# Performance work log

Hardware: AMD Instinct MI355X
Metric: run time of the kernel (lower is better)

Reference implementation:

```python
import jax, jax.numpy as jnp
import numpy as np

B, S, H, NH, HD = 2, 2048, 2048, 16, 128
E, TOPK, I = 8, 2, 2048
EPS = 1e-5
ROPE_THETA = 10000.0


def setup_inputs() -> dict:
    key = jax.random.key(0)
    ks = jax.random.split(key, 11)
    s = 0.02
    return {
        "hidden_states": jax.random.normal(ks[0], (B, S, H), jnp.float32),
        "position_ids": jnp.broadcast_to(jnp.arange(S, dtype=jnp.int32), (B, S)),
        "rms1_w": jnp.ones((H,), jnp.float32),
        "rms2_w": jnp.ones((H,), jnp.float32),
        "q_w": jax.random.normal(ks[1], (H, H), jnp.float32) * s,
        "k_w": jax.random.normal(ks[2], (H, H), jnp.float32) * s,
        "v_w": jax.random.normal(ks[3], (H, H), jnp.float32) * s,
        "o_w": jax.random.normal(ks[4], (H, H), jnp.float32) * s,
        "router_w": jax.random.normal(ks[5], (H, E), jnp.float32) * s,
        "w1": jax.random.normal(ks[6], (E, H, I), jnp.float32) * s,
        "w2": jax.random.normal(ks[7], (E, I, H), jnp.float32) * s,
        "w3": jax.random.normal(ks[8], (E, H, I), jnp.float32) * s,
    }


def rmsnorm(x, w):
    var = jnp.mean(x * x, axis=-1, keepdims=True)
    return (x * jax.lax.rsqrt(var + EPS)) * w


def rope(x, pos):
    # x: [B,S,NH,HD], pos: [B,S]
    half = HD // 2
    inv_freq = 1.0 / (ROPE_THETA ** (jnp.arange(0, half, dtype=jnp.float32) / half))
    ang = pos.astype(jnp.float32)[..., None] * inv_freq  # [B,S,half]
    cos = jnp.cos(ang)[:, :, None, :]
    sin = jnp.sin(ang)[:, :, None, :]
    x1, x2 = x[..., :half], x[..., half:]
    return jnp.concatenate([x1 * cos - x2 * sin, x2 * cos + x1 * sin], axis=-1)


def attention(x, pos, q_w, k_w, v_w, o_w):
    q = (x @ q_w).reshape(B, S, NH, HD)
    k = (x @ k_w).reshape(B, S, NH, HD)
    v = (x @ v_w).reshape(B, S, NH, HD)
    q = rope(q, pos)
    k = rope(k, pos)
    scores = jnp.einsum("bqhd,bkhd->bhqk", q, k) / np.sqrt(HD).astype(np.float32)
    causal = jnp.tril(jnp.ones((S, S), bool))
    scores = jnp.where(causal, scores, jnp.finfo(scores.dtype).min)
    probs = jax.nn.softmax(scores, axis=-1)
    ctx = jnp.einsum("bhqk,bkhd->bqhd", probs, v).reshape(B, S, H)
    return ctx @ o_w


def moe(x, router_w, w1, w2, w3):
    t = x.reshape(B * S, H)
    probs = jax.nn.softmax(t @ router_w, axis=-1)  # [T,E]
    top_v, top_i = jax.lax.top_k(probs, TOPK)
    top_v = top_v / jnp.sum(top_v, axis=-1, keepdims=True)
    T = B * S
    coeff = jnp.zeros((T, E), x.dtype).at[jnp.arange(T)[:, None], top_i].set(top_v)
    y = jnp.zeros((T, H), x.dtype)
    for e in range(E):  # fixed small expert loop
        h = jax.nn.silu(t @ w1[e]) * (t @ w3[e])
        y = y + coeff[:, e:e + 1] * (h @ w2[e])
    return y.reshape(B, S, H)


def reference(hidden_states, position_ids, rms1_w, rms2_w, q_w, k_w, v_w, o_w,
              router_w, w1, w2, w3):
    residual = hidden_states
    h = rmsnorm(hidden_states, rms1_w).astype(hidden_states.dtype)
    h = attention(h, position_ids, q_w, k_w, v_w, o_w)
    h = residual + h
    residual = h
    h = rmsnorm(h, rms2_w).astype(h.dtype)
    h = moe(h, router_w, w1, w2, w3)
    return residual + h
```

## Files before the change

### kernel.cpp

```cpp
#include <hip/hip_runtime.h>
#include <hip/hip_bf16.h>

constexpr int CB   = 2;
constexpr int CS   = 2048;
constexpr int CH   = 2048;
constexpr int CNH  = 16;
constexpr int CHD  = 128;
constexpr int CE   = 8;
constexpr int CI   = 2048;
constexpr int CT   = CB * CS;
constexpr int CQKV = 3 * CH;

typedef __attribute__((ext_vector_type(8))) short short8;
typedef __attribute__((ext_vector_type(4))) float float4v;
typedef __attribute__((ext_vector_type(4))) unsigned short ushort4v;
typedef unsigned int uint32;

__device__ __forceinline__ float bf2f(unsigned short u) {
    union { unsigned int i; float f; } x; x.i = ((unsigned int)u) << 16; return x.f;
}
__device__ __forceinline__ unsigned short f2bf(float f) {
    union { float f; unsigned int i; } x; x.f = f;
    unsigned int r = x.i + 0x7fffu + ((x.i >> 16) & 1u);
    return (unsigned short)(r >> 16);
}
__device__ __forceinline__ uint32 packpair(uint32 r0, uint32 r1) {
    return __builtin_amdgcn_perm(r1, r0, 0x07060302u);
}
__device__ __forceinline__ uint32 rnebits(float f) {
    uint32 u = __float_as_uint(f);
    return u + 0x7fffu + ((u >> 16) & 1u);
}
__device__ __forceinline__ void split2(float f0, float f1, uint32& h, uint32& l) {
    uint32 r0 = rnebits(f0), r1 = rnebits(f1);
    h = packpair(r0, r1);
    float d0 = f0 - __uint_as_float(r0 & 0xffff0000u);
    float d1 = f1 - __uint_as_float(r1 & 0xffff0000u);
    l = packpair(rnebits(d0), rnebits(d1));
}
__device__ __forceinline__ void rne16_store(const float* fv, unsigned short* dst) {
    uint32 h[8];
    #pragma unroll
    for (int p = 0; p < 8; p++) h[p] = packpair(rnebits(fv[2 * p]), rnebits(fv[2 * p + 1]));
    ((uint4*)dst)[0] = make_uint4(h[0], h[1], h[2], h[3]);
    ((uint4*)dst)[1] = make_uint4(h[4], h[5], h[6], h[7]);
}
__device__ __forceinline__ void gl16(const void* g, void* l) {
    __builtin_amdgcn_global_load_lds(
        (const __attribute__((address_space(1))) void*)g,
        (__attribute__((address_space(3))) void*)l, 16, 0, 0);
}

__global__ __launch_bounds__(256) void rmsnorm_k(const float* __restrict__ x,
                                                 const float* __restrict__ w,
                                                 unsigned short* __restrict__ o1,
                                                 unsigned short* __restrict__ o2) {
    const int row = blockIdx.x;
    const float* xr = x + (size_t)row * CH;
    const int base = threadIdx.x * 8;
    float4 v0 = *(const float4*)(xr + base);
    float4 v1 = *(const float4*)(xr + base + 4);
    float ss = v0.x*v0.x + v0.y*v0.y + v0.z*v0.z + v0.w*v0.w
             + v1.x*v1.x + v1.y*v1.y + v1.z*v1.z + v1.w*v1.w;
    #pragma unroll
    for (int o = 1; o < 64; o <<= 1) ss += __shfl_xor(ss, o);
    __shared__ float ps[4];
    if ((threadIdx.x & 63) == 0) ps[threadIdx.x >> 6] = ss;
    __syncthreads();
    const float scale = rsqrtf((ps[0] + ps[1] + ps[2] + ps[3]) / (float)CH + 1e-5f);
    float4 w0 = *(const float4*)(w + base);
    float4 w1 = *(const float4*)(w + base + 4);
    float r[8] = {v0.x * scale * w0.x, v0.y * scale * w0.y, v0.z * scale * w0.z, v0.w * scale * w0.w,
                  v1.x * scale * w1.x, v1.y * scale * w1.y, v1.z * scale * w1.z, v1.w * scale * w1.w};
    uint32 h[4], l[4];
    #pragma unroll
    for (int p = 0; p < 4; p++) split2(r[2 * p], r[2 * p + 1], h[p], l[p]);
    *(uint4*)(o1 + (size_t)row * CH + base) = make_uint4(h[0], h[1], h[2], h[3]);
    *(uint4*)(o2 + (size_t)row * CH + base) = make_uint4(l[0], l[1], l[2], l[3]);
}

__global__ __launch_bounds__(256) void rmsrouter_k(const float* __restrict__ x,
                                                   const float* __restrict__ w,
                                                   const float* __restrict__ rw,
                                                   unsigned short* __restrict__ h2,
                                                   int* __restrict__ cnt,
                                                   int* __restrict__ tok,
                                                   float* __restrict__ gate) {
    const int row = blockIdx.x;
    const float* xr = x + (size_t)row * CH;
    const int base = threadIdx.x * 8;
    float4 v0 = *(const float4*)(xr + base);
    float4 v1 = *(const float4*)(xr + base + 4);
    float ss = v0.x*v0.x + v0.y*v0.y + v0.z*v0.z + v0.w*v0.w
             + v1.x*v1.x + v1.y*v1.y + v1.z*v1.z + v1.w*v1.w;
    #pragma unroll
    for (int o = 1; o < 64; o <<= 1) ss += __shfl_xor(ss, o);
    __shared__ float ps[4];
    __shared__ double dacc[4][8];
    const int wave = threadIdx.x >> 6, lane = threadIdx.x & 63;
    if (lane == 0) ps[wave] = ss;
    __syncthreads();
    const float scale = rsqrtf((ps[0] + ps[1] + ps[2] + ps[3]) / (float)CH + 1e-5f);
    float4 w0 = *(const float4*)(w + base);
    float4 w1 = *(const float4*)(w + base + 4);
    float r[8] = {v0.x * scale * w0.x, v0.y * scale * w0.y, v0.z * scale * w0.z, v0.w * scale * w0.w,
                  v1.x * scale * w1.x, v1.y * scale * w1.y, v1.z * scale * w1.z, v1.w * scale * w1.w};
    rne16_store(r, h2 + (size_t)row * CH + base);
    const float vv[8] = {v0.x, v0.y, v0.z, v0.w, v1.x, v1.y, v1.z, v1.w};
    const float ww[8] = {w0.x, w0.y, w0.z, w0.w, w1.x, w1.y, w1.z, w1.w};
    double acc[8] = {0, 0, 0, 0, 0, 0, 0, 0};
    #pragma unroll
    for (int jj = 0; jj < 8; jj++) {
        const double xn = (double)vv[jj] * (double)ww[jj];
        const float* rr = rw + (size_t)(base + jj) * CE;
        #pragma unroll
        for (int e = 0; e < 8; e++) acc[e] += xn * (double)rr[e];
    }
    #pragma unroll
    for (int e = 0; e < 8; e++) {
        #pragma unroll
        for (int o = 1; o < 64; o <<= 1) acc[e] += __shfl_xor(acc[e], o);
    }
    if (lane == 0) {
        #pragma unroll
        for (int e = 0; e < 8; e++) dacc[wave][e] = acc[e];
    }
    __syncthreads();
    if (threadIdx.x == 0) {
        double a[8];
        #pragma unroll
        for (int e = 0; e < 8; e++) a[e] = dacc[0][e] + dacc[1][e] + dacc[2][e] + dacc[3][e];
        int e0 = 0;
        #pragma unroll
        for (int e = 1; e < 8; e++) if (a[e] > a[e0]) e0 = e;
        int e1 = (e0 == 0) ? 1 : 0;
        #pragma unroll
        for (int e = 0; e < 8; e++) if (e != e0 && a[e] > a[e1]) e1 = e;
        const double dl = (double)scale * (a[e1] - a[e0]);
        const double p1r = exp(dl);
        const float g0 = (float)(1.0 / (1.0 + p1r));
        const float g1 = (float)(p1r / (1.0 + p1r));
        int pos0 = atomicAdd(&cnt[e0], 1);
        tok[e0 * 4096 + pos0] = row; gate[e0 * 4096 + pos0] = g0;
        int pos1 = atomicAdd(&cnt[e1], 1);
        tok[e1 * 4096 + pos1] = row; gate[e1 * 4096 + pos1] = g1;
    }
}

__global__ void rope_tab_k(float2* __restrict__ tab) {
    int i = blockIdx.x * 256 + threadIdx.x;
    int p = i >> 6, j = i & 63;
    double inv = pow(10000.0, -(double)j / 64.0);
    float invf = (float)inv;
    float angf = (float)p * invf;
    double da = (double)angf;
    tab[i] = make_float2((float)cos(da), (float)sin(da));
}

__global__ __launch_bounds__(256) void rope_k(unsigned short* __restrict__ qh,
                                              unsigned short* __restrict__ ql,
                                              const int* __restrict__ pos,
                                              const float2* __restrict__ tab) {
    int i = blockIdx.x * 256 + threadIdx.x;
    if (i >= CT * CNH * 8) return;
    int t = i >> 7, r = i & 127, hh = r >> 3, jo = (r & 7) << 3;
    const float2* tp = tab + (size_t)pos[t] * 64 + jo;
    float4 tc0 = ((const float4*)tp)[0];
    float4 tc1 = ((const float4*)tp)[1];
    float4 tc2 = ((const float4*)tp)[2];
    float4 tc3 = ((const float4*)tp)[3];
    float cx[8] = {tc0.x, tc0.z, tc1.x, tc1.z, tc2.x, tc2.z, tc3.x, tc3.z};
    float cy[8] = {tc0.y, tc0.w, tc1.y, tc1.w, tc2.y, tc2.w, tc3.y, tc3.w};
    const size_t off = (size_t)t * CQKV + hh * CHD + jo;
    #pragma unroll
    for (int s = 0; s < 2; s++) {
        unsigned short* hp = qh + off + s * CH;
        unsigned short* lp = ql + off + s * CH;
        short8 x1h = *(short8*)hp,        x1l = *(short8*)lp;
        short8 x2h = *(short8*)(hp + 64), x2l = *(short8*)(lp + 64);
        const unsigned short* p1h = (const unsigned short*)&x1h;
        const unsigned short* p1l = (const unsigned short*)&x1l;
        const unsigned short* p2h = (const unsigned short*)&x2h;
        const unsigned short* p2l = (const unsigned short*)&x2l;
        short8 y1h, y1l, y2h, y2l;
        unsigned short* q1h = (unsigned short*)&y1h;
        unsigned short* q1l = (unsigned short*)&y1l;
        unsigned short* q2h = (unsigned short*)&y2h;
        unsigned short* q2l = (unsigned short*)&y2l;
        #pragma unroll
        for (int jj = 0; jj < 8; jj++) {
            const float x1 = bf2f(p1h[jj]) + bf2f(p1l[jj]);
            const float x2 = bf2f(p2h[jj]) + bf2f(p2l[jj]);
            const float yy1 = x1 * cx[jj] - x2 * cy[jj];
            const float yy2 = x2 * cx[jj] + x1 * cy[jj];
            const uint32 r1 = rnebits(yy1), r2 = rnebits(yy2);
            q1h[jj] = (unsigned short)(r1 >> 16);
            q2h[jj] = (unsigned short)(r2 >> 16);
            q1l[jj] = f2bf(yy1 - __uint_as_float(r1 & 0xffff0000u));
            q2l[jj] = f2bf(yy2 - __uint_as_float(r2 & 0xffff0000u));
        }
        *(short8*)hp        = y1h;
        *(short8*)(hp + 64) = y2h;
        *(short8*)lp        = y1l;
        *(short8*)(lp + 64) = y2l;
    }
}

template<int NMAT>
__global__ __launch_bounds__(256) void conv_k(const float* __restrict__ S0,
                                              const float* __restrict__ S1,
                                              unsigned short* __restrict__ D) {
    __shared__ float t[64][65];
    const int n0 = blockIdx.x * 64, k0 = blockIdx.y * 64, e = blockIdx.z;
    const size_t esrc = (size_t)e * 2048 * 2048;
    const int cc = threadIdx.x & 63, r4 = threadIdx.x >> 6;
    const int nl = threadIdx.x >> 2, q = threadIdx.x & 3;
    #pragma unroll
    for (int s = 0; s < NMAT; s++) {
        const float* S = s ? S1 : S0;
        __syncthreads();
        #pragma unroll
        for (int j = 0; j < 16; j++) {
            const int row = j * 4 + r4;
            t[cc][row] = S[esrc + (size_t)(k0 + row) * 2048 + n0 + cc];
        }
        __syncthreads();
        const int orow = (NMAT == 2) ? (2 * (n0 + nl) + s) : (n0 + nl);
        unsigned short* dp = D + (size_t)e * (NMAT * 2048) * 2048 + (size_t)orow * 2048 + k0 + q * 16;
        float fv[16];
        #pragma unroll
        for (int j = 0; j < 16; j++) fv[j] = t[nl][q * 16 + j];
        rne16_store(fv, dp);
    }
}

template<int NMAT>
__global__ __launch_bounds__(256) void convs_k(const float* __restrict__ S0,
                                               const float* __restrict__ S1,
                                               const float* __restrict__ S2,
                                               unsigned short* __restrict__ Dh,
                                               unsigned short* __restrict__ Dl) {
    __shared__ float t[64][65];
    const int n0 = blockIdx.x * 64, k0 = blockIdx.y * 64, z = blockIdx.z;
    const float* S = S0;
    if (NMAT == 3) S = (z == 0) ? S0 : ((z == 1) ? S1 : S2);
    const int cc = threadIdx.x & 63, r4 = threadIdx.x >> 6;
    #pragma unroll
    for (int j = 0; j < 16; j++) {
        const int row = j * 4 + r4;
        t[cc][row] = S[(size_t)(k0 + row) * 2048 + n0 + cc];
    }
    __syncthreads();
    const int nl = threadIdx.x >> 2, q = threadIdx.x & 3;
    float fv[16];
    #pragma unroll
    for (int j = 0; j < 16; j++) fv[j] = t[nl][q * 16 + j];
    uint32 h[8], l[8];
    #pragma unroll
    for (int p = 0; p < 8; p++) split2(fv[2 * p], fv[2 * p + 1], h[p], l[p]);
    const size_t off = (size_t)(z * 2048 + n0 + nl) * 2048 + k0 + q * 16;
    ((uint4*)(Dh + off))[0] = make_uint4(h[0], h[1], h[2], h[3]);
    ((uint4*)(Dh + off))[1] = make_uint4(h[4], h[5], h[6], h[7]);
    ((uint4*)(Dl + off))[0] = make_uint4(l[0], l[1], l[2], l[3]);
    ((uint4*)(Dl + off))[1] = make_uint4(l[4], l[5], l[6], l[7]);
}

template<int MODE>
__global__ __launch_bounds__(256) void sgemm_k(
    const unsigned short* __restrict__ Ahg, const unsigned short* __restrict__ Alg, int lda,
    const unsigned short* __restrict__ Bhg, const unsigned short* __restrict__ Blg, int K,
    unsigned short* __restrict__ Ch, unsigned short* __restrict__ Cl,
    float* __restrict__ Cf, int ldc,
    const float* __restrict__ resid, float* __restrict__ C2) {
    __shared__ unsigned short AhS[128 * 32], AlS[128 * 32], BhS[128 * 32], BlS[128 * 32];
    const int mt = blockIdx.x, nt = blockIdx.y, tid = threadIdx.x;
    const int m0 = mt * 128;
    const int wave = tid >> 6, lane = tid & 63;
    const int lr = lane & 15, lg = lane >> 4;
    const int wr = (tid >> 7) & 1, wc = (tid >> 6) & 1;
    const int sr = lane >> 2;
    const int sc = (lane & 3) * 8;
    const int r0 = wave * 32;
    const unsigned short* gAh = Ahg + (size_t)(m0 + r0 + sr) * lda + sc;
    const unsigned short* gAl = Alg + (size_t)(m0 + r0 + sr) * lda + sc;
    const unsigned short* gBh = Bhg + (size_t)(nt * 128 + r0 + sr) * K + sc;
    const unsigned short* gBl = Blg + (size_t)(nt * 128 + r0 + sr) * K + sc;
    const size_t rstepA = (size_t)16 * lda, rstepB = (size_t)16 * K;
    unsigned short* lAh = AhS + r0 * 32;
    unsigned short* lAl = AlS + r0 * 32;
    unsigned short* lBh = BhS + r0 * 32;
    unsigned short* lBl = BlS + r0 * 32;

    float4v acc[4][4];
    #pragma unroll
    for (int m = 0; m < 4; m++)
        #pragma unroll
        for (int n = 0; n < 4; n++) acc[m][n] = (float4v){0.f, 0.f, 0.f, 0.f};

    for (int k0 = 0; k0 < K; k0 += 32) {
        __syncthreads();
        gl16(gAh + k0, lAh);            gl16(gAh + k0 + rstepA, lAh + 512);
        gl16(gAl + k0, lAl);            gl16(gAl + k0 + rstepA, lAl + 512);
        gl16(gBh + k0, lBh);            gl16(gBh + k0 + rstepB, lBh + 512);
        gl16(gBl + k0, lBl);            gl16(gBl + k0 + rstepB, lBl + 512);
        __syncthreads();
        short8 fah[4], fal[4], fbh[4], fbl[4];
        #pragma unroll
        for (int m = 0; m < 4; m++) {
            fah[m] = *(const short8*)(AhS + (wr * 64 + m * 16 + lr) * 32 + lg * 8);
            fal[m] = *(const short8*)(AlS + (wr * 64 + m * 16 + lr) * 32 + lg * 8);
        }
        #pragma unroll
        for (int n = 0; n < 4; n++) {
            fbh[n] = *(const short8*)(BhS + (wc * 64 + n * 16 + lr) * 32 + lg * 8);
            fbl[n] = *(const short8*)(BlS + (wc * 64 + n * 16 + lr) * 32 + lg * 8);
        }
        #pragma unroll
        for (int n = 0; n < 4; n++)
            #pragma unroll
            for (int m = 0; m < 4; m++) {
                acc[m][n] = __builtin_amdgcn_mfma_f32_16x16x32_bf16(fal[m], fbh[n], acc[m][n], 0, 0, 0);
                acc[m][n] = __builtin_amdgcn_mfma_f32_16x16x32_bf16(fah[m], fbl[n], acc[m][n], 0, 0, 0);
                acc[m][n] = __builtin_amdgcn_mfma_f32_16x16x32_bf16(fah[m], fbh[n], acc[m][n], 0, 0, 0);
            }
    }
    #pragma unroll
    for (int m = 0; m < 4; m++) {
        const int rb = wr * 64 + m * 16 + (lane >> 4) * 4;
        #pragma unroll
        for (int n = 0; n < 4; n++) {
            const int ccol = nt * 128 + wc * 64 + n * 16 + lr;
            #pragma unroll
            for (int r = 0; r < 4; r++) {
                const size_t idx = (size_t)(m0 + rb + r) * ldc + ccol;
                if (MODE == 1) {
                    const float v = acc[m][n][r] + resid[idx];
                    Cf[idx] = v;
                    C2[idx] = v;
                } else {
                    const float v = acc[m][n][r];
                    uint32 rr = rnebits(v);
                    Ch[idx] = (unsigned short)(rr >> 16);
                    Cl[idx] = f2bf(v - __uint_as_float(rr & 0xffff0000u));
                }
            }
        }
    }
}

template<int MODE>
__global__ __launch_bounds__(256) void gemm_k(
    const unsigned short* __restrict__ A, int lda,
    const unsigned short* __restrict__ Bt, int K, int Ne,
    void* __restrict__ Cp, int ldc,
    const int* __restrict__ cnt, const int* __restrict__ tokl,
    const float* __restrict__ gatel, const int* __restrict__ pb) {
    __shared__ unsigned short As[128 * 32];
    __shared__ unsigned short Bs[128 * 32];
    const int nt = blockIdx.x, mt = blockIdx.y, e = blockIdx.z;
    const int m0 = mt * 128;
    const int c = cnt[e];
    if (m0 >= c) return;
    const int valid = (c - m0 < 128) ? (c - m0) : 128;
    const int tid = threadIdx.x;
    const int wave = tid >> 6, lane = tid & 63;
    const int lr = lane & 15;
    const int wr = (tid >> 7) & 1, wc = (tid >> 6) & 1;
    const int sr = lane >> 2, sc = (lane & 3) * 8;
    const int r0 = wave * 32;
    size_t gr0, gr1;
    {
        int ra = r0 + sr, rb2 = r0 + 16 + sr;
        if (MODE == 2) {
            ra = ra < valid ? ra : valid - 1;
            rb2 = rb2 < valid ? rb2 : valid - 1;
            gr0 = (size_t)tokl[e * 4096 + m0 + ra];
            gr1 = (size_t)tokl[e * 4096 + m0 + rb2];
        } else {
            int x0 = m0 + ra, x1 = m0 + rb2;
            gr0 = (size_t)(pb[e] + (x0 < c ? x0 : c - 1));
            gr1 = (size_t)(pb[e] + (x1 < c ? x1 : c - 1));
        }
    }
    const unsigned short* gA0 = A + gr0 * (size_t)lda + sc;
    const unsigned short* gA1 = A + gr1 * (size_t)lda + sc;
    const unsigned short* gB = Bt + (size_t)e * Ne * K + (size_t)(nt * 128 + r0 + sr) * K + sc;
    const size_t rstepB = (size_t)16 * K;
    unsigned short* lA = As + r0 * 32;
    unsigned short* lB = Bs + r0 * 32;

    float4v acc[4][4];
    #pragma unroll
    for (int m = 0; m < 4; m++)
        #pragma unroll
        for (int n = 0; n < 4; n++) acc[m][n] = (float4v){0.f, 0.f, 0.f, 0.f};

    for (int k0 = 0; k0 < K; k0 += 32) {
        __syncthreads();
        gl16(gA0 + k0, lA);             gl16(gA1 + k0, lA + 512);
        gl16(gB + k0, lB);              gl16(gB + k0 + rstepB, lB + 512);
        __syncthreads();
        short8 af[4], bf[4];
        const int lg = lane >> 4;
        #pragma unroll
        for (int m = 0; m < 4; m++) af[m] = *(const short8*)(As + (wr * 64 + m * 16 + lr) * 32 + lg * 8);
        #pragma unroll
        for (int n = 0; n < 4; n++) bf[n] = *(const short8*)(Bs + (wc * 64 + n * 16 + lr) * 32 + lg * 8);
        #pragma unroll
        for (int n = 0; n < 4; n++)
            #pragma unroll
            for (int m = 0; m < 4; m++)
                acc[m][n] = __builtin_amdgcn_mfma_f32_16x16x32_bf16(af[m], bf[n], acc[m][n], 0, 0, 0);
    }

    #pragma unroll
    for (int m = 0; m < 4; m++) {
        const int rb = wr * 64 + m * 16 + (lane >> 4) * 4;
        #pragma unroll
        for (int n = 0; n < 4; n++) {
            const int col = nt * 128 + wc * 64 + n * 16 + lr;
            #pragma unroll
            for (int r = 0; r < 4; r++) {
                const int row = rb + r;
                const float v = acc[m][n][r];
                if (MODE == 2) {
                    const float other = __shfl_xor(v, 1);
                    if (!(lr & 1) && row < valid) {
                        const float g1 = v, g3 = other;
                        const float hsw = (g1 / (1.f + __expf(-g1))) * g3;
                        ((unsigned short*)Cp)[(size_t)(pb[e] + m0 + row) * ldc + (col >> 1)] = f2bf(hsw);
                    }
                } else {
                    if (row < valid) {
                        const int t = tokl[e * 4096 + m0 + row];
                        const float g = gatel[e * 4096 + m0 + row];
                        atomicAdd(((float*)Cp) + (size_t)t * ldc + col, v * g);
                    }
                }
            }
        }
    }
}

__global__ __launch_bounds__(256) void attn_k(const unsigned short* __restrict__ qh,
                                              const unsigned short* __restrict__ ql,
                                              unsigned short* __restrict__ ch,
                                              unsigned short* __restrict__ cl) {
    __shared__ unsigned short Ksh[32][136], Ksl[32][136];
    __shared__ unsigned short Vth[128][40], Vtl[128][40];
    const int bid = blockIdx.x;
    const int xcd = bid & 7, jj = bid >> 3;
    const int bh  = xcd * 4 + (jj >> 5);
    const int qb  = 31 - (jj & 31);
    const int h   = bh & 15, b = bh >> 4;
    const int tid = threadIdx.x;
    const int wave = tid >> 6, lane = tid & 63, lr = lane & 15, lg = lane >> 4;
    const size_t tb = (size_t)b * CS;
    const int q0 = qb * 64 + wave * 16;

    short8 qfh[4], qfl[4];
    {
        const size_t off = (tb + q0 + lr) * CQKV + h * CHD;
        #pragma unroll
        for (int c = 0; c < 4; c++) {
            qfh[c] = *(const short8*)(qh + off + c * 32 + lg * 8);
            qfl[c] = *(const short8*)(ql + off + c * 32 + lg * 8);
        }
    }
    float4v o[8];
    #pragma unroll
    for (int d = 0; d < 8; d++) o[d] = (float4v){0.f, 0.f, 0.f, 0.f};
    float m = -1e30f, l = 0.f;
    const float scl = 0.08838834764831845f;
    const int ntiles = 2 * (qb + 1);
    const int kk = tid >> 3, slot = tid & 7;
    const int vd = tid & 127, vhalf = tid >> 7;

    short8 pkh0, pkh1, pkl0, pkl1;
    unsigned short pth[16], ptl[16];
    {
        const size_t koff = (tb + kk) * CQKV + CH + h * CHD + slot * 16;
        pkh0 = *(const short8*)(qh + koff);
        pkh1 = *(const short8*)(qh + koff + 8);
        pkl0 = *(const short8*)(ql + koff);
        pkl1 = *(const short8*)(ql + koff + 8);
        const size_t voff = (tb + vhalf * 16) * CQKV + 2 * CH + h * CHD + vd;
        #pragma unroll
        for (int j = 0; j < 16; j++) {
            pth[j] = qh[voff + (size_t)j * CQKV];
            ptl[j] = ql[voff + (size_t)j * CQKV];
        }
    }

    for (int kt = 0; kt < ntiles; ++kt) {
        const int kv0 = kt * 32;
        __syncthreads();
        *(short8*)(&Ksh[kk][slot * 16])     = pkh0;
        *(short8*)(&Ksh[kk][slot * 16 + 8]) = pkh1;
        *(short8*)(&Ksl[kk][slot * 16])     = pkl0;
        *(short8*)(&Ksl[kk][slot * 16 + 8]) = pkl1;
        #pragma unroll
        for (int p = 0; p < 2; p++) {
            *(ushort4v*)(&Vth[vd][vhalf * 16 + p * 8])     = *(ushort4v*)(&pth[p * 8]);
            *(ushort4v*)(&Vth[vd][vhalf * 16 + p * 8 + 4]) = *(ushort4v*)(&pth[p * 8 + 4]);
            *(ushort4v*)(&Vtl[vd][vhalf * 16 + p * 8])     = *(ushort4v*)(&ptl[p * 8]);
            *(ushort4v*)(&Vtl[vd][vhalf * 16 + p * 8 + 4]) = *(ushort4v*)(&ptl[p * 8 + 4]);
        }
        if (kt + 1 < ntiles) {
            const int nv0 = kv0 + 32;
            const size_t koff = (tb + nv0 + kk) * CQKV + CH + h * CHD + slot * 16;
            pkh0 = *(const short8*)(qh + koff);
            pkh1 = *(const short8*)(qh + koff + 8);
            pkl0 = *(const short8*)(ql + koff);
            pkl1 = *(const short8*)(ql + koff + 8);
            const size_t voff = (tb + nv0 + vhalf * 16) * CQKV + 2 * CH + h * CHD + vd;
            #pragma unroll
            for (int j = 0; j < 16; j++) {
                pth[j] = qh[voff + (size_t)j * CQKV];
                ptl[j] = ql[voff + (size_t)j * CQKV];
            }
        }
        __syncthreads();

        float4v st0 = (float4v){0.f,0.f,0.f,0.f}, st1 = st0;
        #pragma unroll
        for (int c = 0; c < 4; c++) {
            short8 kah = *(const short8*)(&Ksh[lr][c * 32 + lg * 8]);
            short8 kal = *(const short8*)(&Ksl[lr][c * 32 + lg * 8]);
            short8 kbh = *(const short8*)(&Ksh[16 + lr][c * 32 + lg * 8]);
            short8 kbl = *(const short8*)(&Ksl[16 + lr][c * 32 + lg * 8]);
            st0 = __builtin_amdgcn_mfma_f32_16x16x32_bf16(kal, qfh[c], st0, 0, 0, 0);
            st0 = __builtin_amdgcn_mfma_f32_16x16x32_bf16(kah, qfl[c], st0, 0, 0, 0);
            st0 = __builtin_amdgcn_mfma_f32_16x16x32_bf16(kah, qfh[c], st0, 0, 0, 0);
            st1 = __builtin_amdgcn_mfma_f32_16x16x32_bf16(kbl, qfh[c], st1, 0, 0, 0);
            st1 = __builtin_amdgcn_mfma_f32_16x16x32_bf16(kbh, qfl[c], st1, 0, 0, 0);
            st1 = __builtin_amdgcn_mfma_f32_16x16x32_bf16(kbh, qfh[c], st1, 0, 0, 0);
        }
        float pv[8]; float pmax = -1e30f;
        const int qg = q0 + lr;
        #pragma unroll
        for (int f = 0; f < 2; f++) {
            #pragma unroll
            for (int r = 0; r < 4; r++) {
                const int kg = kv0 + f * 16 + lg * 4 + r;
                const float s = (kg <= qg) ? ((f ? st1[r] : st0[r]) * scl) : -1e30f;
                pv[f * 4 + r] = s;
                pmax = fmaxf(pmax, s);
            }
        }
        pmax = fmaxf(pmax, __shfl_xor(pmax, 16));
        pmax = fmaxf(pmax, __shfl_xor(pmax, 32));
        if (!__all(pmax <= m)) {
            const float mnew = fmaxf(m, pmax);
            const float alpha = __expf(m - mnew);
            l *= alpha;
            #pragma unroll
            for (int d = 0; d < 8; d++) o[d] *= alpha;
            m = mnew;
        }
        float sum = 0.f;
        #pragma unroll
        for (int i = 0; i < 8; i++) { const float p = __expf(pv[i] - m); pv[i] = p; sum += p; }
        sum += __shfl_xor(sum, 16);
        sum += __shfl_xor(sum, 32);
        l += sum;
        short8 pfh, pfl;
        unsigned short* pfhp = (unsigned short*)&pfh;
        unsigned short* pflp = (unsigned short*)&pfl;
        #pragma unroll
        for (int j = 0; j < 8; j++) {
            const int srcl = (((lg & 1) * 2 + (j >> 2)) << 4) | lr;
            const float a0 = __shfl(pv[j & 3], srcl);
            const float a1 = __shfl(pv[4 + (j & 3)], srcl);
            const float sel = (lg >= 2) ? a1 : a0;
            uint32 r = rnebits(sel);
            pfhp[j] = (unsigned short)(r >> 16);
            float d = sel - __uint_as_float(r & 0xffff0000u);
            pflp[j] = (unsigned short)(rnebits(d) >> 16);
        }
        #pragma unroll
        for (int dt = 0; dt < 8; dt++) {
            short8 vh = *(const short8*)(&Vth[dt * 16 + lr][lg * 8]);
            short8 vl = *(const short8*)(&Vtl[dt * 16 + lr][lg * 8]);
            o[dt] = __builtin_amdgcn_mfma_f32_16x16x32_bf16(vl, pfh, o[dt], 0, 0, 0);
            o[dt] = __builtin_amdgcn_mfma_f32_16x16x32_bf16(vh, pfl, o[dt], 0, 0, 0);
            o[dt] = __builtin_amdgcn_mfma_f32_16x16x32_bf16(vh, pfh, o[dt], 0, 0, 0);
        }
    }
    const float inv = 1.f / l;
    const size_t coff = (tb + q0 + lr) * CH + h * CHD + lg * 4;
    #pragma unroll
    for (int dt = 0; dt < 8; dt++) {
        ushort4v wh, wl;
        #pragma unroll
        for (int r = 0; r < 4; r++) {
            const float v = o[dt][r] * inv;
            uint32 rr = rnebits(v);
            wh[r] = (unsigned short)(rr >> 16);
            wl[r] = f2bf(v - __uint_as_float(rr & 0xffff0000u));
        }
        *(ushort4v*)(ch + coff + dt * 16) = wh;
        *(ushort4v*)(cl + coff + dt * 16) = wl;
    }
}

__global__ void prefix_k(const int* __restrict__ cnt, int* __restrict__ pb) {
    if (threadIdx.x == 0 && blockIdx.x == 0) {
        int s = 0;
        for (int e = 0; e < CE; e++) { pb[e] = s; s += cnt[e]; }
    }
}

extern "C" void kernel_launch(void* const* d_in, const int* in_sizes, int n_in,
                              void* d_out, int out_size, void* d_ws, size_t ws_size,
                              hipStream_t stream) {
    (void)in_sizes; (void)n_in; (void)out_size; (void)ws_size;
    const float* hidden = (const float*)d_in[0];
    const int*   posids = (const int*)d_in[1];
    const float* rms1w  = (const float*)d_in[2];
    const float* rms2w  = (const float*)d_in[3];
    const float* qw     = (const float*)d_in[4];
    const float* kw     = (const float*)d_in[5];
    const float* vw     = (const float*)d_in[6];
    const float* ow     = (const float*)d_in[7];
    const float* rw     = (const float*)d_in[8];
    const float* w1     = (const float*)d_in[9];
    const float* w2     = (const float*)d_in[10];
    const float* w3     = (const float*)d_in[11];
    float* out = (float*)d_out;

    char* ws = (char*)d_ws;
    unsigned short* h1h = (unsigned short*)ws;
    unsigned short* h1l = (unsigned short*)(ws + 16777216);
    unsigned short* woh = (unsigned short*)ws;
    unsigned short* wol = (unsigned short*)(ws + 8388608);
    unsigned short* h2  = (unsigned short*)ws;
    int*   tok  = (int*)(ws + 16777216);
    float* gate = (float*)(ws + 16777216 + 131072);
    int*   cnt  = (int*)(ws + 16777216 + 262144);
    int*   pb   = cnt + 16;
    unsigned short* qkvh = (unsigned short*)(ws + 33554432);
    unsigned short* qkvl = (unsigned short*)(ws + 83886080);
    unsigned short* wt13 = (unsigned short*)(ws + 33554432);
    unsigned short* wt2  = (unsigned short*)(ws + 33554432);
    unsigned short* wqkvh = (unsigned short*)(ws + 134217728);
    unsigned short* wqkvl = (unsigned short*)(ws + 134217728 + 25165824);
    unsigned short* ctxh = (unsigned short*)(ws + 134217728);
    unsigned short* ctxl = (unsigned short*)(ws + 150994944);
    float*          res2 = (float*)(ws + 167772160);
    unsigned short* Hbuf = (unsigned short*)(ws + 167772160);
    float2*         rtab = (float2*)(ws + 201326592);

    rope_tab_k<<<512, 256, 0, stream>>>(rtab);
    rmsnorm_k<<<CT, 256, 0, stream>>>(hidden, rms1w, h1h, h1l);
    convs_k<3><<<dim3(32, 32, 3), 256, 0, stream>>>(qw, kw, vw, wqkvh, wqkvl);
    sgemm_k<0><<<dim3(32, 48), 256, 0, stream>>>(h1h, h1l, CH, wqkvh, wqkvl, CH,
                                                 qkvh, qkvl, nullptr, CQKV, nullptr, nullptr);
    rope_k<<<2048, 256, 0, stream>>>(qkvh, qkvl, posids, rtab);
    convs_k<1><<<dim3(32, 32, 1), 256, 0, stream>>>(ow, nullptr, nullptr, woh, wol);
    attn_k<<<1024, 256, 0, stream>>>(qkvh, qkvl, ctxh, ctxl);
    sgemm_k<1><<<dim3(32, 16), 256, 0, stream>>>(ctxh, ctxl, CH, woh, wol, CH,
                                                 nullptr, nullptr, res2, CH, hidden, out);
    hipMemsetAsync(cnt, 0, 8 * sizeof(int), stream);
    rmsrouter_k<<<CT, 256, 0, stream>>>(res2, rms2w, rw, h2, cnt, tok, gate);
    prefix_k<<<1, 64, 0, stream>>>(cnt, pb);
    conv_k<2><<<dim3(32, 32, CE), 256, 0, stream>>>(w1, w3, wt13);
    gemm_k<2><<<dim3(32, 32, CE), 256, 0, stream>>>(h2, CH, wt13, CH, 2 * CI, Hbuf, CI,
                                                    cnt, tok, gate, pb);
    conv_k<1><<<dim3(32, 32, CE), 256, 0, stream>>>(w2, nullptr, wt2);
    gemm_k<3><<<dim3(16, 32, CE), 256, 0, stream>>>(Hbuf, CI, wt2, CI, CH, out, CH,
                                                    cnt, tok, gate, pb);
}
```

Measured before the change: 1.382 ms.

## Double-buffer LDS tiles in split-bf16 and MoE GEMM kernels

Both GEMM kernels now keep two LDS stages. The next K-slice is loaded into one stage while MFMAs run on the other, with one barrier per iteration instead of two. The goal is to hide global-to-LDS load latency behind compute. This doubles LDS use per block (64KB for the split kernel), which may cut occupancy. It also relies on gl16's completion semantics being correctly synchronised by the single barrier.

```diff
diff --git a/kernel.cpp b/kernel.cpp
--- a/kernel.cpp
+++ b/kernel.cpp
@@ -272,7 +272,7 @@
     unsigned short* __restrict__ Ch, unsigned short* __restrict__ Cl,
     float* __restrict__ Cf, int ldc,
     const float* __restrict__ resid, float* __restrict__ C2) {
-    __shared__ unsigned short AhS[128 * 32], AlS[128 * 32], BhS[128 * 32], BlS[128 * 32];
+    __shared__ unsigned short SS[2][4][128 * 32];
     const int mt = blockIdx.x, nt = blockIdx.y, tid = threadIdx.x;
     const int m0 = mt * 128;
     const int wave = tid >> 6, lane = tid & 63;
@@ -281,15 +281,12 @@
     const int sr = lane >> 2;
     const int sc = (lane & 3) * 8;
     const int r0 = wave * 32;
+    const int lofs = r0 * 32;
     const unsigned short* gAh = Ahg + (size_t)(m0 + r0 + sr) * lda + sc;
     const unsigned short* gAl = Alg + (size_t)(m0 + r0 + sr) * lda + sc;
     const unsigned short* gBh = Bhg + (size_t)(nt * 128 + r0 + sr) * K + sc;
     const unsigned short* gBl = Blg + (size_t)(nt * 128 + r0 + sr) * K + sc;
     const size_t rstepA = (size_t)16 * lda, rstepB = (size_t)16 * K;
-    unsigned short* lAh = AhS + r0 * 32;
-    unsigned short* lAl = AlS + r0 * 32;
-    unsigned short* lBh = BhS + r0 * 32;
-    unsigned short* lBl = BlS + r0 * 32;
 
     float4v acc[4][4];
     #pragma unroll
@@ -297,23 +294,36 @@
         #pragma unroll
         for (int n = 0; n < 4; n++) acc[m][n] = (float4v){0.f, 0.f, 0.f, 0.f};
 
+    gl16(gAh, &SS[0][0][lofs]);           gl16(gAh + rstepA, &SS[0][0][lofs + 512]);
+    gl16(gAl, &SS[0][1][lofs]);           gl16(gAl + rstepA, &SS[0][1][lofs + 512]);
+    gl16(gBh, &SS[0][2][lofs]);           gl16(gBh + rstepB, &SS[0][2][lofs + 512]);
+    gl16(gBl, &SS[0][3][lofs]);           gl16(gBl + rstepB, &SS[0][3][lofs + 512]);
+    __syncthreads();
+
+    int cur = 0;
     for (int k0 = 0; k0 < K; k0 += 32) {
-        __syncthreads();
-        gl16(gAh + k0, lAh);            gl16(gAh + k0 + rstepA, lAh + 512);
-        gl16(gAl + k0, lAl);            gl16(gAl + k0 + rstepA, lAl + 512);
-        gl16(gBh + k0, lBh);            gl16(gBh + k0 + rstepB, lBh + 512);
-        gl16(gBl + k0, lBl);            gl16(gBl + k0 + rstepB, lBl + 512);
-        __syncthreads();
+        if (k0 + 32 < K) {
+            const int nb = cur ^ 1;
+            const int kn = k0 + 32;
+            gl16(gAh + kn, &SS[nb][0][lofs]);          gl16(gAh + kn + rstepA, &SS[nb][0][lofs + 512]);
+            gl16(gAl + kn, &SS[nb][1][lofs]);          gl16(gAl + kn + rstepA, &SS[nb][1][lofs + 512]);
+            gl16(gBh + kn, &SS[nb][2][lofs]);          gl16(gBh + kn + rstepB, &SS[nb][2][lofs + 512]);
+            gl16(gBl + kn, &SS[nb][3][lofs]);          gl16(gBl + kn + rstepB, &SS[nb][3][lofs + 512]);
+        }
+        const unsigned short* PAh = SS[cur][0];
+        const unsigned short* PAl = SS[cur][1];
+        const unsigned short* PBh = SS[cur][2];
+        const unsigned short* PBl = SS[cur][3];
         short8 fah[4], fal[4], fbh[4], fbl[4];
         #pragma unroll
         for (int m = 0; m < 4; m++) {
-            fah[m] = *(const short8*)(AhS + (wr * 64 + m * 16 + lr) * 32 + lg * 8);
-            fal[m] = *(const short8*)(AlS + (wr * 64 + m * 16 + lr) * 32 + lg * 8);
+            fah[m] = *(const short8*)(PAh + (wr * 64 + m * 16 + lr) * 32 + lg * 8);
+            fal[m] = *(const short8*)(PAl + (wr * 64 + m * 16 + lr) * 32 + lg * 8);
         }
         #pragma unroll
         for (int n = 0; n < 4; n++) {
-            fbh[n] = *(const short8*)(BhS + (wc * 64 + n * 16 + lr) * 32 + lg * 8);
-            fbl[n] = *(const short8*)(BlS + (wc * 64 + n * 16 + lr) * 32 + lg * 8);
+            fbh[n] = *(const short8*)(PBh + (wc * 64 + n * 16 + lr) * 32 + lg * 8);
+            fbl[n] = *(const short8*)(PBl + (wc * 64 + n * 16 + lr) * 32 + lg * 8);
         }
         #pragma unroll
         for (int n = 0; n < 4; n++)
@@ -323,6 +333,8 @@
                 acc[m][n] = __builtin_amdgcn_mfma_f32_16x16x32_bf16(fah[m], fbl[n], acc[m][n], 0, 0, 0);
                 acc[m][n] = __builtin_amdgcn_mfma_f32_16x16x32_bf16(fah[m], fbh[n], acc[m][n], 0, 0, 0);
             }
+        __syncthreads();
+        cur ^= 1;
     }
     #pragma unroll
     for (int m = 0; m < 4; m++) {
@@ -355,8 +367,7 @@
     void* __restrict__ Cp, int ldc,
     const int* __restrict__ cnt, const int* __restrict__ tokl,
     const float* __restrict__ gatel, const int* __restrict__ pb) {
-    __shared__ unsigned short As[128 * 32];
-    __shared__ unsigned short Bs[128 * 32];
+    __shared__ unsigned short SS[2][2][128 * 32];
     const int nt = blockIdx.x, mt = blockIdx.y, e = blockIdx.z;
     const int m0 = mt * 128;
     const int c = cnt[e];
@@ -368,6 +379,7 @@
     const int wr = (tid >> 7) & 1, wc = (tid >> 6) & 1;
     const int sr = lane >> 2, sc = (lane & 3) * 8;
     const int r0 = wave * 32;
+    const int lofs = r0 * 32;
     size_t gr0, gr1;
     {
         int ra = r0 + sr, rb2 = r0 + 16 + sr;
@@ -386,8 +398,6 @@
     const unsigned short* gA1 = A + gr1 * (size_t)lda + sc;
     const unsigned short* gB = Bt + (size_t)e * Ne * K + (size_t)(nt * 128 + r0 + sr) * K + sc;
     const size_t rstepB = (size_t)16 * K;
-    unsigned short* lA = As + r0 * 32;
-    unsigned short* lB = Bs + r0 * 32;
 
     float4v acc[4][4];
     #pragma unroll
@@ -395,22 +405,33 @@
         #pragma unroll
         for (int n = 0; n < 4; n++) acc[m][n] = (float4v){0.f, 0.f, 0.f, 0.f};
 
+    gl16(gA0, &SS[0][0][lofs]);           gl16(gA1, &SS[0][0][lofs + 512]);
+    gl16(gB, &SS[0][1][lofs]);            gl16(gB + rstepB, &SS[0][1][lofs + 512]);
+    __syncthreads();
+
+    int cur = 0;
     for (int k0 = 0; k0 < K; k0 += 32) {
-        __syncthreads();
-        gl16(gA0 + k0, lA);             gl16(gA1 + k0, lA + 512);
-        gl16(gB + k0, lB);              gl16(gB + k0 + rstepB, lB + 512);
-        __syncthreads();
+        if (k0 + 32 < K) {
+            const int nb = cur ^ 1;
+            const int kn = k0 + 32;
+            gl16(gA0 + kn, &SS[nb][0][lofs]);          gl16(gA1 + kn, &SS[nb][0][lofs + 512]);
+            gl16(gB + kn, &SS[nb][1][lofs]);           gl16(gB + kn + rstepB, &SS[nb][1][lofs + 512]);
+        }
+        const unsigned short* PA = SS[cur][0];
+        const unsigned short* PB = SS[cur][1];
         short8 af[4], bf[4];
         const int lg = lane >> 4;
         #pragma unroll
-        for (int m = 0; m < 4; m++) af[m] = *(const short8*)(As + (wr * 64 + m * 16 + lr) * 32 + lg * 8);
-        #pragma unroll
-        for (int n = 0; n < 4; n++) bf[n] = *(const short8*)(Bs + (wc * 64 + n * 16 + lr) * 32 + lg * 8);
+        for (int m = 0; m < 4; m++) af[m] = *(const short8*)(PA + (wr * 64 + m * 16 + lr) * 32 + lg * 8);
+        #pragma unroll
+        for (int n = 0; n < 4; n++) bf[n] = *(const short8*)(PB + (wc * 64 + n * 16 + lr) * 32 + lg * 8);
         #pragma unroll
         for (int n = 0; n < 4; n++)
             #pragma unroll
             for (int m = 0; m < 4; m++)
                 acc[m][n] = __builtin_amdgcn_mfma_f32_16x16x32_bf16(af[m], bf[n], acc[m][n], 0, 0, 0);
+        __syncthreads();
+        cur ^= 1;
     }
 
     #pragma unroll
```

Measured after the change: 1.315 ms. -4.9%, faster.
